# Performance work log

Hardware: AMD Instinct MI355X
Metric: run time of the kernel (lower is better)

The kernel has to match this reference:

```python
import jax, jax.numpy as jnp
import numpy as np

NUM_GROUPS = 8
NUM_HEADS = 4
EPS = 1e-5


def group_norm(x, w, b):
    # x: [B, C, H, W]; normalize over (C/G, H, W) within each of G groups
    B, C, H, W = x.shape
    xg = x.reshape(B, NUM_GROUPS, C // NUM_GROUPS, H, W)
    mean = xg.mean(axis=(2, 3, 4), keepdims=True)
    var = xg.var(axis=(2, 3, 4), keepdims=True)
    xn = ((xg - mean) * jax.lax.rsqrt(var + EPS)).reshape(B, C, H, W)
    return xn * w[None, :, None, None] + b[None, :, None, None]


def setup_inputs() -> dict:
    key = jax.random.key(0)
    ks = jax.random.split(key, 7)
    B, C, H, W = 4, 256, 64, 64
    x = jax.random.normal(ks[0], (B, C, H, W), dtype=jnp.float32)
    gn_w = jax.random.normal(ks[1], (C,), dtype=jnp.float32) * 0.1 + 1.0
    gn_b = jax.random.normal(ks[2], (C,), dtype=jnp.float32) * 0.1
    qkv_w = jax.random.normal(ks[3], (3 * C, C), dtype=jnp.float32) / np.sqrt(C)
    qkv_b = jax.random.normal(ks[4], (3 * C,), dtype=jnp.float32) * 0.02
    proj_w = jax.random.normal(ks[5], (C, C), dtype=jnp.float32) / np.sqrt(C)
    proj_b = jax.random.normal(ks[6], (C,), dtype=jnp.float32) * 0.02
    return {"x": x, "gn_w": gn_w, "gn_b": gn_b, "qkv_w": qkv_w,
            "qkv_b": qkv_b, "proj_w": proj_w, "proj_b": proj_b}


def reference(x, gn_w, gn_b, qkv_w, qkv_b, proj_w, proj_b):
    B, C, H, W = x.shape
    nh = NUM_HEADS
    hd = C // nh
    scale = hd ** -0.5
    N = H * W

    h = group_norm(x, gn_w, gn_b)
    # 1x1 conv == channel matmul: [B, 3C, H, W]
    qkv = jnp.einsum('oc,bchw->bohw', qkv_w, h) + qkv_b[None, :, None, None]
    qkv = qkv.reshape(B, 3, nh, hd, N)  # matches torch .view(B,3,nh,hd,HW)
    q, k, v = qkv[:, 0], qkv[:, 1], qkv[:, 2]  # each [B, nh, hd, N]

    attn = jnp.einsum('bhdn,bhdm->bhnm', q, k) * scale  # [B, nh, N, N]
    attn = jax.nn.softmax(attn, axis=-1)
    out = jnp.einsum('bhnm,bhdm->bhdn', attn, v)  # [B, nh, hd, N]
    out = out.reshape(B, C, H, W)

    proj = jnp.einsum('oc,bchw->bohw', proj_w, out) + proj_b[None, :, None, None]
    return x + proj
```

## Files before the change

kernel.cpp:

```cpp
#include <hip/hip_runtime.h>
#include <hip/hip_bf16.h>

#define BB   4
#define CC   256
#define NN   4096
#define NH   4
#define HD   64
#define NG   8
#define GSZ  32
#define EPSV 1e-5f
#define SCALE_L2E 0.18033688f

typedef __bf16 bf16x8 __attribute__((ext_vector_type(8)));
typedef float  f32x4  __attribute__((ext_vector_type(4)));

#define MFMA16(a, b, c)  __builtin_amdgcn_mfma_f32_16x16x32_bf16((a), (b), (c), 0, 0, 0)

#if __has_builtin(__builtin_amdgcn_exp2f)
#define EXP2F __builtin_amdgcn_exp2f
#else
#define EXP2F exp2f
#endif

#define WAITV(n)  asm volatile("s_waitcnt vmcnt(" #n ")" ::: "memory")
#define WAITL0    asm volatile("s_waitcnt lgkmcnt(0)" ::: "memory")
#define SBAR      __builtin_amdgcn_s_barrier()
#define SCHED0    __builtin_amdgcn_sched_barrier(0)

__device__ inline unsigned short f2bf(float f) {
    unsigned int u = __float_as_uint(f);
    u += 0x7fffu + ((u >> 16) & 1u);
    return (unsigned short)(u >> 16);
}

__device__ __forceinline__ bf16x8 pk8(const f32x4& p0, const f32x4& p1) {
    alignas(16) unsigned int u[4];
    u[0] = __builtin_amdgcn_perm(__float_as_uint(p0[1]), __float_as_uint(p0[0]), 0x07060302u);
    u[1] = __builtin_amdgcn_perm(__float_as_uint(p0[3]), __float_as_uint(p0[2]), 0x07060302u);
    u[2] = __builtin_amdgcn_perm(__float_as_uint(p1[1]), __float_as_uint(p1[0]), 0x07060302u);
    u[3] = __builtin_amdgcn_perm(__float_as_uint(p1[3]), __float_as_uint(p1[2]), 0x07060302u);
    return *reinterpret_cast<bf16x8*>(u);
}

__device__ __forceinline__ void async_ld16(void* lds, const void* g) {
    __builtin_amdgcn_global_load_lds(
        (const __attribute__((address_space(1))) unsigned int*)g,
        (__attribute__((address_space(3))) unsigned int*)lds, 16, 0, 0);
}

__global__ void k_prep(const float* __restrict__ x, float* __restrict__ stats,
                       const float* __restrict__ wp, unsigned short* __restrict__ op) {
    int blk = blockIdx.x;
    int t = threadIdx.x;
    if (blk >= 256) {
        int i = (blk - 256) * 256 + t;
        if (i < CC * CC) op[i] = f2bf(wp[i]);
        return;
    }
    int b = blk >> 6, g = (blk >> 3) & 7, s = blk & 7;
    const float* p = x + ((size_t)(b * CC + g * GSZ)) * NN + s * 16384;
    float s0 = 0.f, s1 = 0.f;
    #pragma unroll
    for (int i = 0; i < 64; ++i) { float v = p[i * 256 + t]; s0 += v; s1 += v * v; }
    #pragma unroll
    for (int m = 1; m <= 32; m <<= 1) { s0 += __shfl_xor(s0, m); s1 += __shfl_xor(s1, m); }
    __shared__ float ls[8];
    int w = t >> 6;
    if ((t & 63) == 0) { ls[w * 2] = s0; ls[w * 2 + 1] = s1; }
    __syncthreads();
    if (t == 0) {
        float a0 = ls[0] + ls[2] + ls[4] + ls[6];
        float a1 = ls[1] + ls[3] + ls[5] + ls[7];
        atomicAdd(&stats[(b * NG + g) * 2 + 0], a0);
        atomicAdd(&stats[(b * NG + g) * 2 + 1], a1);
    }
}

__global__ void __launch_bounds__(256)
k_tab(const float* __restrict__ wq, const float* __restrict__ gw, const float* __restrict__ gb,
      const float* __restrict__ qb, const float* __restrict__ stats,
      unsigned short* __restrict__ wqp, float* __restrict__ biasq) {
    int o = blockIdx.x, b = blockIdx.y, c = threadIdx.x;
    float s0 = stats[(b * NG + (c >> 5)) * 2 + 0];
    float s1 = stats[(b * NG + (c >> 5)) * 2 + 1];
    float mean = s0 * (1.0f / 131072.0f);
    float var  = s1 * (1.0f / 131072.0f) - mean * mean;
    float inv  = rsqrtf(var + EPSV);
    float Ac = gw[c] * inv;
    float Bc = gb[c] - mean * Ac;
    float w = wq[o * CC + c];
    wqp[((size_t)b * 768 + o) * CC + c] = f2bf(w * Ac);
    float p = w * Bc;
    #pragma unroll
    for (int m = 1; m <= 32; m <<= 1) p += __shfl_xor(p, m);
    __shared__ float ls[4];
    if ((c & 63) == 0) ls[c >> 6] = p;
    __syncthreads();
    if (c == 0) biasq[b * 768 + o] = qb[o] + ls[0] + ls[1] + ls[2] + ls[3];
}

__global__ void __launch_bounds__(256)
k_qkv(const float* __restrict__ x, const unsigned short* __restrict__ wqp,
      const float* __restrict__ biasq,
      unsigned short* __restrict__ qt, unsigned short* __restrict__ kt,
      unsigned short* __restrict__ vt) {
    int bx = blockIdx.x, by = blockIdx.y;
    int t = threadIdx.x, wave = t >> 6, lane = t & 63;
    int l15 = lane & 15, quad = lane >> 4;
    int wm = wave >> 1, wn = wave & 1;

    __shared__ alignas(16) unsigned char smem[49152];

    int nn0 = bx * 128;
    int b = nn0 >> 12, nbase = nn0 & 4095;

    const char* Ag = (const char*)wqp + (size_t)b * 393216 + (size_t)by * 65536;
    int row0 = t >> 2, slot = t & 3;
    size_t a0 = (size_t)row0 * 512 + slot * 16;
    size_t a1 = a0 + 64 * 512;
    unsigned int dstA = wave * 1024;

    int colsrc = (((lane & 31) * 16) - 32 * wave) & 511;
    const char* xrow = (const char*)x +
        (((size_t)(b * CC) + (wave * 8 + (lane >> 5))) * NN + nbase) * 4 + colsrc;

    auto stage = [&](int buf, int kk) {
        async_ld16(smem + buf * 8192 + dstA,        Ag + a0 + (size_t)kk * 64);
        async_ld16(smem + buf * 8192 + 4096 + dstA, Ag + a1 + (size_t)kk * 64);
        const char* bs = xrow + (size_t)kk * 32 * NN * 4;
        unsigned char* bd = smem + 16384 + buf * 16384 + wave * 4096;
        async_ld16(bd,        bs);
        async_ld16(bd + 1024, bs + (size_t)2 * NN * 4);
        async_ld16(bd + 2048, bs + (size_t)4 * NN * 4);
        async_ld16(bd + 3072, bs + (size_t)6 * NN * 4);
    };

    int colr[4];
    #pragma unroll
    for (int f = 0; f < 4; ++f)
        colr[f] = (((wn * 64 + f * 16 + l15) * 4) + quad * 32) & 511;

    f32x4 acc[4][4];
    #pragma unroll
    for (int i = 0; i < 4; ++i)
        #pragma unroll
        for (int j = 0; j < 4; ++j) acc[i][j] = (f32x4){0.f, 0.f, 0.f, 0.f};

    stage(0, 0);
    stage(1, 1);

    for (int kk = 0; kk < 8; ++kk) {
        if (kk < 7) { WAITV(6); } else { WAITV(0); }
        SCHED0;
        SBAR;
        SCHED0;
        int cur = kk & 1;
        bf16x8 af[4], bf[4];
        #pragma unroll
        for (int f = 0; f < 4; ++f)
            af[f] = *reinterpret_cast<const bf16x8*>(smem + cur * 8192 + (wm * 64 + f * 16 + l15) * 64 + quad * 16);
        #pragma unroll
        for (int f = 0; f < 4; ++f) {
            const unsigned char* fb = smem + 16384 + cur * 16384 + quad * 4096 + colr[f];
            alignas(16) unsigned int u[4];
            #pragma unroll
            for (int jj = 0; jj < 4; ++jj) {
                float xl = *reinterpret_cast<const float*>(fb + (2 * jj) * 512);
                float xh = *reinterpret_cast<const float*>(fb + (2 * jj + 1) * 512);
                asm("v_cvt_pk_bf16_f32 %0, %1, %2" : "=v"(u[jj]) : "v"(xl), "v"(xh));
            }
            bf[f] = *reinterpret_cast<const bf16x8*>(u);
        }
        #pragma unroll
        for (int fm = 0; fm < 4; ++fm)
            #pragma unroll
            for (int fn = 0; fn < 4; ++fn)
                acc[fm][fn] = MFMA16(af[fm], bf[fn], acc[fm][fn]);
        WAITL0;
        SCHED0;
        SBAR;
        SCHED0;
        if (kk < 6) stage(cur, kk + 2);
    }

    int s = by >> 1;
    if (s < 2) {
        #pragma unroll
        for (int fm = 0; fm < 4; ++fm) {
            int o = by * 128 + wm * 64 + fm * 16 + quad * 4;
            int h = (o >> 6) & 3, d0 = o & 63;
            float bias[4];
            #pragma unroll
            for (int r = 0; r < 4; ++r) bias[r] = biasq[b * 768 + o + r];
            #pragma unroll
            for (int fn = 0; fn < 4; ++fn) {
                int n = nbase + wn * 64 + fn * 16 + l15;
                alignas(8) unsigned short o4[4];
                if (s == 0) {
                    #pragma unroll
                    for (int r = 0; r < 4; ++r) o4[r] = f2bf((acc[fm][fn][r] + bias[r]) * SCALE_L2E);
                    *reinterpret_cast<uint2*>(qt + (((size_t)(b * NH + h) * NN) + n) * HD + d0) =
                        *reinterpret_cast<const uint2*>(o4);
                } else {
                    #pragma unroll
                    for (int r = 0; r < 4; ++r) o4[r] = f2bf(acc[fm][fn][r] + bias[r]);
                    *reinterpret_cast<uint2*>(kt + (((size_t)(b * NH + h) * NN) + n) * HD + d0) =
                        *reinterpret_cast<const uint2*>(o4);
                }
            }
        }
    } else {
        unsigned short* vtile = (unsigned short*)smem;
        #pragma unroll
        for (int fm = 0; fm < 4; ++fm) {
            int o  = by * 128 + wm * 64 + fm * 16 + quad * 4;
            int ol = wm * 64 + fm * 16 + quad * 4;
            float bias[4];
            #pragma unroll
            for (int r = 0; r < 4; ++r) bias[r] = biasq[b * 768 + o + r];
            #pragma unroll
            for (int fn = 0; fn < 4; ++fn) {
                int nl = wn * 64 + fn * 16 + l15;
                #pragma unroll
                for (int r = 0; r < 4; ++r)
                    vtile[(ol + r) * 132 + nl] = f2bf(acc[fm][fn][r] + bias[r]);
            }
        }
        __syncthreads();
        int hbase = (by - 4) * 2;
        #pragma unroll
        for (int pass = 0; pass < 8; ++pass) {
            int row  = pass * 16 + (t >> 4);
            int col0 = (t & 15) * 8;
            int nb = (col0 & ~31) | ((col0 & 16) >> 1) | ((col0 & 8) >> 1);
            const unsigned short* src = vtile + row * 132 + nb;
            uint2 lo = *reinterpret_cast<const uint2*>(src);
            uint2 hi = *reinterpret_cast<const uint2*>(src + 16);
            uint4 o4 = make_uint4(lo.x, lo.y, hi.x, hi.y);
            int h = hbase + (row >> 6), d = row & 63;
            *reinterpret_cast<uint4*>(vt + ((size_t)(b * NH + h) * HD + d) * NN + nbase + col0) = o4;
        }
    }
}

__global__ void __launch_bounds__(256, 4)
k_attn(const unsigned short* __restrict__ qt, const unsigned short* __restrict__ kt,
       const unsigned short* __restrict__ vt,
       unsigned short* __restrict__ op0, unsigned short* __restrict__ op1,
       float* __restrict__ lip) {
    int bh = blockIdx.y;
    int split = blockIdx.z;
    int t = threadIdx.x, wave = t >> 6, lane = t & 63;
    int l15 = lane & 15, quad = lane >> 4;
    int qbase = blockIdx.x * 128 + wave * 32;
    int kbase = split * 2048;
    const unsigned short* qp = qt + (size_t)bh * NN * HD;
    const unsigned short* kp = kt + (size_t)bh * NN * HD;
    const unsigned short* vp = vt + (size_t)bh * HD * NN;

    __shared__ alignas(16) unsigned char kbuf[2][8192];
    __shared__ alignas(16) unsigned char vbuf[2][8192];

    int lr8 = lane >> 3, lc8 = lane & 7;
    int swz = lc8 ^ lr8;
    const char* ksrc = (const char*)kp + (size_t)(kbase + wave * 16 + lr8) * 128 + swz * 16;
    const char* vsrc = (const char*)vp + (size_t)(wave * 16 + lr8) * 8192 + (size_t)kbase * 2 + swz * 16;
    unsigned int dstw = wave * 2048;

    auto stage = [&](int buf) {
        async_ld16(kbuf[buf] + dstw,        ksrc);
        async_ld16(kbuf[buf] + dstw + 1024, ksrc + 1024);
        ksrc += 8192;
        async_ld16(vbuf[buf] + dstw,        vsrc);
        async_ld16(vbuf[buf] + dstw + 1024, vsrc + 8 * 8192);
        vsrc += 128;
    };

    bf16x8 qaA0 = *reinterpret_cast<const bf16x8*>(qp + (size_t)(qbase + l15) * HD + quad * 8);
    bf16x8 qaA1 = *reinterpret_cast<const bf16x8*>(qp + (size_t)(qbase + l15) * HD + 32 + quad * 8);
    bf16x8 qaB0 = *reinterpret_cast<const bf16x8*>(qp + (size_t)(qbase + 16 + l15) * HD + quad * 8);
    bf16x8 qaB1 = *reinterpret_cast<const bf16x8*>(qp + (size_t)(qbase + 16 + l15) * HD + 32 + quad * 8);

    const f32x4 Z4 = (f32x4){0.f, 0.f, 0.f, 0.f};
    bf16x8 vone;
    #pragma unroll
    for (int i = 0; i < 8; ++i) vone[i] = (__bf16)1.0f;

    f32x4 OA[4], OB[4];
    #pragma unroll
    for (int i = 0; i < 4; ++i) { OA[i] = Z4; OB[i] = Z4; }
    f32x4 liAA = Z4, liBB = Z4;

    int sx = l15 & 7;

    auto compute = [&](const unsigned char* kb, const unsigned char* vbb) {
        f32x4 sA0[2], sA1[2], sB0[2], sB1[2];
        __builtin_amdgcn_s_setprio(1);
        #pragma unroll
        for (int s = 0; s < 2; ++s) {
            int r0 = (s * 32 + l15) * 128;
            bf16x8 k00 = *reinterpret_cast<const bf16x8*>(kb + r0 + ((quad ^ sx) * 16));
            bf16x8 k01 = *reinterpret_cast<const bf16x8*>(kb + r0 + (((quad + 4) ^ sx) * 16));
            bf16x8 k10 = *reinterpret_cast<const bf16x8*>(kb + r0 + 2048 + ((quad ^ sx) * 16));
            bf16x8 k11 = *reinterpret_cast<const bf16x8*>(kb + r0 + 2048 + (((quad + 4) ^ sx) * 16));
            sA0[s] = MFMA16(k00, qaA0, Z4);  sA0[s] = MFMA16(k01, qaA1, sA0[s]);
            sA1[s] = MFMA16(k10, qaA0, Z4);  sA1[s] = MFMA16(k11, qaA1, sA1[s]);
            sB0[s] = MFMA16(k00, qaB0, Z4);  sB0[s] = MFMA16(k01, qaB1, sB0[s]);
            sB1[s] = MFMA16(k10, qaB0, Z4);  sB1[s] = MFMA16(k11, qaB1, sB1[s]);
        }
        __builtin_amdgcn_s_setprio(0);
        #pragma unroll
        for (int s = 0; s < 2; ++s) {
            f32x4 pA0, pA1, pB0, pB1;
            #pragma unroll
            for (int r = 0; r < 4; ++r) {
                pA0[r] = EXP2F(sA0[s][r]);  pA1[r] = EXP2F(sA1[s][r]);
                pB0[r] = EXP2F(sB0[s][r]);  pB1[r] = EXP2F(sB1[s][r]);
            }
            bf16x8 fA = pk8(pA0, pA1);
            bf16x8 fB = pk8(pB0, pB1);

            __builtin_amdgcn_s_setprio(1);
            liAA = MFMA16(fA, vone, liAA);
            liBB = MFMA16(fB, vone, liBB);

            #pragma unroll
            for (int dc = 0; dc < 4; ++dc) {
                const unsigned char* vrow = vbb + (dc * 16 + l15) * 128;
                bf16x8 vv = *reinterpret_cast<const bf16x8*>(vrow + (((s * 4 + quad) ^ sx) * 16));
                OA[dc] = MFMA16(fA, vv, OA[dc]);
                OB[dc] = MFMA16(fB, vv, OB[dc]);
            }
            __builtin_amdgcn_s_setprio(0);
        }
    };

    stage(0);
    __syncthreads();

    for (int p = 0; p < 16; ++p) {
        stage(1);
        compute(kbuf[0], vbuf[0]);
        __syncthreads();
        if (p < 15) stage(0);
        compute(kbuf[1], vbuf[1]);
        __syncthreads();
    }

    unsigned short* op = split ? op1 : op0;
    int b = bh >> 2, h = bh & 3;
    #pragma unroll
    for (int dc = 0; dc < 4; ++dc) {
        #pragma unroll
        for (int r = 0; r < 4; ++r) {
            int qA = qbase + quad * 4 + r;
            op[((size_t)(b * NN) + qA) * CC + h * HD + dc * 16 + l15]      = f2bf(OA[dc][r]);
            op[((size_t)(b * NN) + qA + 16) * CC + h * HD + dc * 16 + l15] = f2bf(OB[dc][r]);
        }
    }
    float* lp = lip + (size_t)split * (16 * NN) + (size_t)bh * NN + qbase;
    if (l15 == 0) {
        #pragma unroll
        for (int r = 0; r < 4; ++r) {
            lp[quad * 4 + r]      = liAA[r];
            lp[16 + quad * 4 + r] = liBB[r];
        }
    }
}

__global__ void __launch_bounds__(256)
k_proj(const unsigned short* __restrict__ ao, const unsigned short* __restrict__ p1,
       const float* __restrict__ lip,
       const unsigned short* __restrict__ wp, const float* __restrict__ pb,
       const float* __restrict__ x, float* __restrict__ out) {
    int bx = blockIdx.x, by = blockIdx.y;
    int t = threadIdx.x, wave = t >> 6, lane = t & 63;
    int l15 = lane & 15, quad = lane >> 4;
    int wm = wave >> 1, wn = wave & 1;

    __shared__ alignas(16) unsigned char At[2][4096];
    __shared__ alignas(16) unsigned char Bt[2][4096];

    const char* Ag = (const char*)wp + (size_t)by * 32768;
    int row0 = t >> 2, slot = t & 3;
    size_t a0 = (size_t)row0 * 512 + slot * 16;
    unsigned int dst0 = wave * 1024;

    int gtok = bx * 64 + row0;
    int b = gtok >> 12, n = gtok & 4095;
    size_t obase = ((size_t)(b * NN) + n) * CC + slot * 8;
    float inv[4];
    #pragma unroll
    for (int h = 0; h < 4; ++h) {
        size_t lb = (size_t)(b * 4 + h) * NN + n;
        inv[h] = 1.0f / (lip[lb] + lip[lb + (size_t)16 * NN]);
    }

    auto stageA = [&](int buf, int kk) {
        async_ld16(At[buf] + dst0, Ag + a0 + (size_t)kk * 64);
    };
    uint4 eu0, eu1, ou0, ou1;
    auto loadB = [&](uint4& r0, uint4& r1, int kk) {
        r0 = *reinterpret_cast<const uint4*>(ao + obase + kk * 32);
        r1 = *reinterpret_cast<const uint4*>(p1 + obase + kk * 32);
    };
    auto writeB = [&](int buf, const uint4& r0, const uint4& r1, float iv) {
        const unsigned short* q0 = reinterpret_cast<const unsigned short*>(&r0);
        const unsigned short* q1 = reinterpret_cast<const unsigned short*>(&r1);
        alignas(16) unsigned short o8[8];
        #pragma unroll
        for (int i = 0; i < 8; ++i) {
            float f0 = __uint_as_float((unsigned)q0[i] << 16);
            float f1 = __uint_as_float((unsigned)q1[i] << 16);
            o8[i] = f2bf((f0 + f1) * iv);
        }
        *reinterpret_cast<uint4*>(Bt[buf] + row0 * 64 + slot * 16) =
            *reinterpret_cast<const uint4*>(o8);
    };

    f32x4 acc[2][2];
    #pragma unroll
    for (int i = 0; i < 2; ++i)
        #pragma unroll
        for (int j = 0; j < 2; ++j) acc[i][j] = (f32x4){0.f, 0.f, 0.f, 0.f};

    loadB(eu0, eu1, 0);
    stageA(0, 0);
    loadB(ou0, ou1, 1);

    #pragma unroll
    for (int k2 = 0; k2 < 4; ++k2) {
        {
            const int kk = 2 * k2;
            WAITV(2);
            SCHED0;
            writeB(0, eu0, eu1, inv[kk >> 1]);
            WAITL0;
            SCHED0;
            SBAR;
            SCHED0;
            if (kk < 7) stageA(1, kk + 1);
            if (kk < 6) loadB(eu0, eu1, kk + 2);
            bf16x8 af[2], bf[2];
            #pragma unroll
            for (int f = 0; f < 2; ++f) {
                af[f] = *reinterpret_cast<const bf16x8*>(At[0] + (wm * 32 + f * 16 + l15) * 64 + quad * 16);
                bf[f] = *reinterpret_cast<const bf16x8*>(Bt[0] + (wn * 32 + f * 16 + l15) * 64 + quad * 16);
            }
            #pragma unroll
            for (int fm = 0; fm < 2; ++fm)
                #pragma unroll
                for (int fn = 0; fn < 2; ++fn)
                    acc[fm][fn] = MFMA16(af[fm], bf[fn], acc[fm][fn]);
        }
        {
            const int kk = 2 * k2 + 1;
            if (kk < 7) { WAITV(2); } else { WAITV(0); }
            SCHED0;
            writeB(1, ou0, ou1, inv[kk >> 1]);
            WAITL0;
            SCHED0;
            SBAR;
            SCHED0;
            if (kk < 7) stageA(0, kk + 1);
            if (kk < 6) loadB(ou0, ou1, kk + 2);
            bf16x8 af[2], bf[2];
            #pragma unroll
            for (int f = 0; f < 2; ++f) {
                af[f] = *reinterpret_cast<const bf16x8*>(At[1] + (wm * 32 + f * 16 + l15) * 64 + quad * 16);
                bf[f] = *reinterpret_cast<const bf16x8*>(Bt[1] + (wn * 32 + f * 16 + l15) * 64 + quad * 16);
            }
            #pragma unroll
            for (int fm = 0; fm < 2; ++fm)
                #pragma unroll
                for (int fn = 0; fn < 2; ++fn)
                    acc[fm][fn] = MFMA16(af[fm], bf[fn], acc[fm][fn]);
        }
    }

    int nn0 = bx * 64;
    int bb = nn0 >> 12, nbase = nn0 & 4095;
    #pragma unroll
    for (int fm = 0; fm < 2; ++fm) {
        int o = by * 64 + wm * 32 + fm * 16 + quad * 4;
        float bias[4];
        #pragma unroll
        for (int r = 0; r < 4; ++r) bias[r] = pb[o + r];
        #pragma unroll
        for (int fn = 0; fn < 2; ++fn) {
            int nc = nbase + wn * 32 + fn * 16 + l15;
            #pragma unroll
            for (int r = 0; r < 4; ++r) {
                size_t idx = ((size_t)(bb * CC + o + r)) * NN + nc;
                out[idx] = acc[fm][fn][r] + bias[r] + x[idx];
            }
        }
    }
}

extern "C" void kernel_launch(void* const* d_in, const int* in_sizes, int n_in,
                              void* d_out, int out_size, void* d_ws, size_t ws_size,
                              hipStream_t stream) {
    const float* x     = (const float*)d_in[0];
    const float* gw    = (const float*)d_in[1];
    const float* gb    = (const float*)d_in[2];
    const float* qkvw  = (const float*)d_in[3];
    const float* qkvb  = (const float*)d_in[4];
    const float* projw = (const float*)d_in[5];
    const float* projb = (const float*)d_in[6];
    float* out = (float*)d_out;

    char* w = (char*)d_ws;
    size_t off = 0;
    unsigned short* qt = (unsigned short*)(w + off); off += (size_t)BB * NH * NN * HD * 2;
    unsigned short* kt = (unsigned short*)(w + off); off += (size_t)BB * NH * NN * HD * 2;
    unsigned short* vt = (unsigned short*)(w + off); off += (size_t)BB * NH * HD * NN * 2;
    unsigned short* ao = (unsigned short*)(w + off); off += (size_t)BB * NN * CC * 2;
    unsigned short* pt1 = (unsigned short*)(w + off); off += (size_t)BB * NN * CC * 2;
    unsigned short* wqp = (unsigned short*)(w + off); off += (size_t)BB * 3 * CC * CC * 2;
    float* biasq = (float*)(w + off); off += (size_t)BB * 3 * CC * sizeof(float);
    unsigned short* wpb = (unsigned short*)(w + off); off += (size_t)CC * CC * 2;
    float* stats = (float*)(w + off); off += BB * NG * 2 * sizeof(float);
    float* lip   = (float*)(w + off); off += (size_t)2 * 16 * NN * sizeof(float);

    hipMemsetAsync(stats, 0, BB * NG * 2 * sizeof(float), stream);
    k_prep<<<512, 256, 0, stream>>>(x, stats, projw, wpb);
    k_tab<<<dim3(3 * CC, BB), 256, 0, stream>>>(qkvw, gw, gb, qkvb, stats, wqp, biasq);
    k_qkv<<<dim3(BB * NN / 128, 6), 256, 0, stream>>>(x, wqp, biasq, qt, kt, vt);
    k_attn<<<dim3(NN / 128, BB * NH, 2), 256, 0, stream>>>(qt, kt, vt, ao, pt1, lip);
    k_proj<<<dim3(BB * NN / 64, CC / 64), 256, 0, stream>>>(ao, pt1, lip, wpb, projb, x, out);
}
```

Measured before the change: 185.4 us.

## Load V fragments directly from global memory instead of staging through LDS

```diff
diff --git a/kernel.cpp b/kernel.cpp
--- a/kernel.cpp
+++ b/kernel.cpp
@@ -259,22 +259,22 @@
     const unsigned short* vp = vt + (size_t)bh * HD * NN;
 
     __shared__ alignas(16) unsigned char kbuf[2][8192];
-    __shared__ alignas(16) unsigned char vbuf[2][8192];
 
     int lr8 = lane >> 3, lc8 = lane & 7;
     int swz = lc8 ^ lr8;
     const char* ksrc = (const char*)kp + (size_t)(kbase + wave * 16 + lr8) * 128 + swz * 16;
-    const char* vsrc = (const char*)vp + (size_t)(wave * 16 + lr8) * 8192 + (size_t)kbase * 2 + swz * 16;
     unsigned int dstw = wave * 2048;
 
     auto stage = [&](int buf) {
         async_ld16(kbuf[buf] + dstw,        ksrc);
         async_ld16(kbuf[buf] + dstw + 1024, ksrc + 1024);
         ksrc += 8192;
-        async_ld16(vbuf[buf] + dstw,        vsrc);
-        async_ld16(vbuf[buf] + dstw + 1024, vsrc + 8 * 8192);
-        vsrc += 128;
     };
+
+    const char* vr0 = (const char*)vp + (size_t)l15 * 8192 + (size_t)kbase * 2 + quad * 16;
+    const char* vr1 = vr0 + (size_t)16 * 8192;
+    const char* vr2 = vr0 + (size_t)32 * 8192;
+    const char* vr3 = vr0 + (size_t)48 * 8192;
 
     bf16x8 qaA0 = *reinterpret_cast<const bf16x8*>(qp + (size_t)(qbase + l15) * HD + quad * 8);
     bf16x8 qaA1 = *reinterpret_cast<const bf16x8*>(qp + (size_t)(qbase + l15) * HD + 32 + quad * 8);
@@ -293,7 +293,17 @@
 
     int sx = l15 & 7;
 
-    auto compute = [&](const unsigned char* kb, const unsigned char* vbb) {
+    auto compute = [&](const unsigned char* kb) {
+        bf16x8 v00 = *reinterpret_cast<const bf16x8*>(vr0);
+        bf16x8 v01 = *reinterpret_cast<const bf16x8*>(vr1);
+        bf16x8 v02 = *reinterpret_cast<const bf16x8*>(vr2);
+        bf16x8 v03 = *reinterpret_cast<const bf16x8*>(vr3);
+        bf16x8 v10 = *reinterpret_cast<const bf16x8*>(vr0 + 64);
+        bf16x8 v11 = *reinterpret_cast<const bf16x8*>(vr1 + 64);
+        bf16x8 v12 = *reinterpret_cast<const bf16x8*>(vr2 + 64);
+        bf16x8 v13 = *reinterpret_cast<const bf16x8*>(vr3 + 64);
+        vr0 += 128; vr1 += 128; vr2 += 128; vr3 += 128;
+
         f32x4 sA0[2], sA1[2], sB0[2], sB1[2];
         __builtin_amdgcn_s_setprio(1);
         #pragma unroll
@@ -324,12 +334,16 @@
             liAA = MFMA16(fA, vone, liAA);
             liBB = MFMA16(fB, vone, liBB);
 
-            #pragma unroll
-            for (int dc = 0; dc < 4; ++dc) {
-                const unsigned char* vrow = vbb + (dc * 16 + l15) * 128;
-                bf16x8 vv = *reinterpret_cast<const bf16x8*>(vrow + (((s * 4 + quad) ^ sx) * 16));
-                OA[dc] = MFMA16(fA, vv, OA[dc]);
-                OB[dc] = MFMA16(fB, vv, OB[dc]);
+            if (s == 0) {
+                OA[0] = MFMA16(fA, v00, OA[0]);  OB[0] = MFMA16(fB, v00, OB[0]);
+                OA[1] = MFMA16(fA, v01, OA[1]);  OB[1] = MFMA16(fB, v01, OB[1]);
+                OA[2] = MFMA16(fA, v02, OA[2]);  OB[2] = MFMA16(fB, v02, OB[2]);
+                OA[3] = MFMA16(fA, v03, OA[3]);  OB[3] = MFMA16(fB, v03, OB[3]);
+            } else {
+                OA[0] = MFMA16(fA, v10, OA[0]);  OB[0] = MFMA16(fB, v10, OB[0]);
+                OA[1] = MFMA16(fA, v11, OA[1]);  OB[1] = MFMA16(fB, v11, OB[1]);
+                OA[2] = MFMA16(fA, v12, OA[2]);  OB[2] = MFMA16(fB, v12, OB[2]);
+                OA[3] = MFMA16(fA, v13, OA[3]);  OB[3] = MFMA16(fB, v13, OB[3]);
             }
             __builtin_amdgcn_s_setprio(0);
         }
@@ -340,10 +354,10 @@
 
     for (int p = 0; p < 16; ++p) {
         stage(1);
-        compute(kbuf[0], vbuf[0]);
+        compute(kbuf[0]);
         __syncthreads();
         if (p < 15) stage(0);
-        compute(kbuf[1], vbuf[1]);
+        compute(kbuf[1]);
         __syncthreads();
     }
 
```

Result: slower. 364.1 us (+96.4%).
